# Performance work log

Measured on AMD Instinct MI355X. Metric: run time of the kernel, lower is better.

Reference implementation:

```python
import jax, jax.numpy as jnp
import numpy as np

N, H = 8192, 1024

def setup_inputs() -> dict:
    key = jax.random.key(0)
    ks = jax.random.split(key, 7)
    s = 1.0 / np.sqrt(H)
    return {
        "x": jax.random.normal(ks[0], (N, H), dtype=jnp.float32),
        "Wq": jax.random.uniform(ks[1], (H, H), dtype=jnp.float32, minval=-s, maxval=s),
        "bq": jax.random.uniform(ks[2], (H,), dtype=jnp.float32, minval=-s, maxval=s),
        "Wk": jax.random.uniform(ks[3], (H, H), dtype=jnp.float32, minval=-s, maxval=s),
        "bk": jax.random.uniform(ks[4], (H,), dtype=jnp.float32, minval=-s, maxval=s),
        "Wv": jax.random.uniform(ks[5], (H, H), dtype=jnp.float32, minval=-s, maxval=s),
        "bv": jax.random.uniform(ks[6], (H,), dtype=jnp.float32, minval=-s, maxval=s),
    }

def reference(x, Wq, bq, Wk, bk, Wv, bv):
    # q/k/v projections: [N, H]
    q = x @ Wq + bq
    k = x @ Wk + bk
    v = x @ Wv + bv
    # full scores [N, N]; NOTE: original has no 1/sqrt(d) scaling
    scores = q @ k.T
    alpha = jax.nn.softmax(scores, axis=1)
    return alpha @ v
```

## Files before the change

kernel.cpp:

```cpp
#include <hip/hip_runtime.h>
#include <hip/hip_bf16.h>
#include <hip/hip_fp16.h>


typedef _Float16 f16x8 __attribute__((ext_vector_type(8)));
typedef float floatx4 __attribute__((ext_vector_type(4)));
typedef float floatx2 __attribute__((ext_vector_type(2)));
typedef unsigned short ushortx8 __attribute__((ext_vector_type(8)));

__device__ __forceinline__ unsigned short f2h(float f) {
  __half h = __float2half(f);
  return __builtin_bit_cast(unsigned short, h);
}
__device__ __forceinline__ float h2f(unsigned short u) {
  return __half2float(__builtin_bit_cast(__half, u));
}

__device__ __forceinline__ void async16(const void* g, void* l) {
  __builtin_amdgcn_global_load_lds(
      (__attribute__((address_space(1))) unsigned int*)(g),
      (__attribute__((address_space(3))) unsigned int*)(l),
      16, 0, 0);
}


__global__ __launch_bounds__(256) void conv_f32_f16(const float* __restrict__ in,
                                                    unsigned short* __restrict__ out,
                                                    long n) {
  long i = ((long)blockIdx.x * 256 + threadIdx.x) * 4;
  if (i + 3 < n) {
    float4 f = *(const float4*)(in + i);
    ushort4 o;
    o.x = f2h(f.x); o.y = f2h(f.y); o.z = f2h(f.z); o.w = f2h(f.w);
    *(ushort4*)(out + i) = o;
  }
}

__global__ __launch_bounds__(256) void transpose_f32_f16_3(const float* __restrict__ in0,
                                                           const float* __restrict__ in1,
                                                           const float* __restrict__ in2,
                                                           unsigned short* __restrict__ out,
                                                           int rows, int cols) {
  const float* in = (blockIdx.z == 0) ? in0 : (blockIdx.z == 1) ? in1 : in2;
  unsigned short* o = out + (size_t)blockIdx.z * rows * cols;
  __shared__ float tile[32][33];
  int bx = blockIdx.x * 32;
  int by = blockIdx.y * 32;
  int tx = threadIdx.x & 31, ty = threadIdx.x >> 5;
  #pragma unroll
  for (int yy = ty; yy < 32; yy += 8)
    tile[yy][tx] = in[(size_t)(by + yy) * cols + bx + tx];
  __syncthreads();
  #pragma unroll
  for (int yy = ty; yy < 32; yy += 8)
    o[(size_t)(bx + yy) * rows + by + tx] = f2h(tile[tx][yy]);
}

__global__ __launch_bounds__(256, 4)
void gemm_bt(const unsigned short* __restrict__ A,
             const unsigned short* __restrict__ B,
             int M, int Nn, int K,
             const float* __restrict__ b0, const float* __restrict__ b1,
             const float* __restrict__ b2,
             unsigned short* __restrict__ out) {
  B   += (size_t)blockIdx.z * Nn * K;
  out += (size_t)blockIdx.z * M * Nn;
  const float* bias = (blockIdx.z == 0) ? b0 : (blockIdx.z == 1) ? b1 : b2;
  __shared__ unsigned short smem[128 * 136];
  unsigned short* As = smem;
  unsigned short* Bs = smem + 128 * 32;
  const int tid  = threadIdx.x;
  const int wave = tid >> 6;
  const int lane = tid & 63;
  const int wm = wave >> 1, wn = wave & 1;
  const int quad = lane >> 4, l16 = lane & 15;
  const long bm = (long)blockIdx.y * 128;
  const long bn = (long)blockIdx.x * 128;

  floatx4 acc[4][4] = {};

  const int srow = wave * 32 + (lane >> 2);
  const int scol = (lane & 3) * 8;
  const unsigned short* gA0 = A + (bm + srow) * (long)K + scol;
  const unsigned short* gA1 = gA0 + 16L * K;
  const unsigned short* gB0 = B + (bn + srow) * (long)K + scol;
  const unsigned short* gB1 = gB0 + 16L * K;
  unsigned short* lA0 = &As[(wave * 32) * 32];
  unsigned short* lA1 = &As[(wave * 32 + 16) * 32];
  unsigned short* lB0 = &Bs[(wave * 32) * 32];
  unsigned short* lB1 = &Bs[(wave * 32 + 16) * 32];

  for (int kk = 0; kk < K; kk += 32) {
    async16(gA0 + kk, lA0);
    async16(gA1 + kk, lA1);
    async16(gB0 + kk, lB0);
    async16(gB1 + kk, lB1);
    __syncthreads();
    f16x8 af[4], bfv[4];
    #pragma unroll
    for (int i = 0; i < 4; ++i) {
      af[i]  = *reinterpret_cast<const f16x8*>(&As[(wm * 64 + i * 16 + l16) * 32 + quad * 8]);
      bfv[i] = *reinterpret_cast<const f16x8*>(&Bs[(wn * 64 + i * 16 + l16) * 32 + quad * 8]);
    }
    #pragma unroll
    for (int i = 0; i < 4; ++i)
      #pragma unroll
      for (int j = 0; j < 4; ++j)
        acc[i][j] = __builtin_amdgcn_mfma_f32_16x16x32_f16(af[i], bfv[j], acc[i][j], 0, 0, 0);
    __syncthreads();
  }
  #pragma unroll
  for (int i = 0; i < 4; ++i) {
    const int row0 = wm * 64 + i * 16 + quad * 4;
    #pragma unroll
    for (int j = 0; j < 4; ++j) {
      const int col = wn * 64 + j * 16 + l16;
      const float cb = bias[bn + col];
      #pragma unroll
      for (int r = 0; r < 4; ++r)
        smem[(row0 + r) * 136 + col] = f2h(acc[i][j][r] + cb);
    }
  }
  __syncthreads();
  #pragma unroll
  for (int u = 0; u < 8; ++u) {
    const int chunk = u * 256 + tid;
    const int row = chunk >> 4;
    const int cc = chunk & 15;
    const ushortx8 val = *reinterpret_cast<const ushortx8*>(&smem[row * 136 + cc * 8]);
    *reinterpret_cast<ushortx8*>(&out[(bm + row) * (long)Nn + bn + cc * 8]) = val;
  }
}

__global__ __launch_bounds__(512, 2)
void gemm256(const unsigned short* __restrict__ A,
             const unsigned short* __restrict__ B,
             unsigned short* __restrict__ out) {
  constexpr int Nd = 8192;
  constexpr int K = 1024;
  __shared__ unsigned short smem[65536];
  const int tid  = threadIdx.x;
  const int lane = tid & 63;
  const int wave = tid >> 6;
  const int wm = wave >> 2, wn = wave & 3;
  const int quad = lane >> 4, l16 = lane & 15;

  const unsigned lin = blockIdx.y * gridDim.x + blockIdx.x;
  const unsigned nb  = gridDim.x * gridDim.y;
  const unsigned swz = (lin & 7u) * (nb >> 3) + (lin >> 3);
  const long bm = (long)(swz >> 5) * 256;
  const long bn = (long)(swz & 31u) * 256;

  floatx4 acc[8][4] = {};

  const int c0 = tid, c1 = tid + 512;
  const int r0 = c0 >> 2, r1 = c1 >> 2;
  const int sl0 = (c0 & 3) ^ ((r0 >> 1) & 3);
  const int sl1 = (c1 & 3) ^ ((r1 >> 1) & 3);
  const unsigned short* gA0 = A + (bm + r0) * (long)K + sl0 * 8;
  const unsigned short* gA1 = A + (bm + r1) * (long)K + sl1 * 8;
  const unsigned short* gB0 = B + (bn + r0) * (long)K + sl0 * 8;
  const unsigned short* gB1 = B + (bn + r1) * (long)K + sl1 * 8;
  const int ldsw0 = (c0 & ~63) * 8;
  const int ldsw1 = (c1 & ~63) * 8;

  auto STAGE = [&](int kt) {
    unsigned short* bufA = smem + (kt & 3) * 16384;
    unsigned short* bufB = bufA + 8192;
    const int ko = kt * 32;
    async16(gA0 + ko, bufA + ldsw0);
    async16(gA1 + ko, bufA + ldsw1);
    async16(gB0 + ko, bufB + ldsw0);
    async16(gB1 + ko, bufB + ldsw1);
  };

  STAGE(0); STAGE(1); STAGE(2);

  for (int kt = 0; kt < 32; ++kt) {
    const unsigned short* bufA = smem + (kt & 3) * 16384;
    const unsigned short* bufB = bufA + 8192;
    if (kt <= 29)      asm volatile("s_waitcnt vmcnt(8)" ::: "memory");
    else if (kt == 30) asm volatile("s_waitcnt vmcnt(4)" ::: "memory");
    else               asm volatile("s_waitcnt vmcnt(0)" ::: "memory");
    __builtin_amdgcn_s_barrier();
    __builtin_amdgcn_sched_barrier(0);
    if (kt + 3 < 32) STAGE(kt + 3);

    f16x8 bf[4];
    #pragma unroll
    for (int j = 0; j < 4; ++j) {
      const int R = wn * 64 + j * 16 + l16;
      bf[j] = *reinterpret_cast<const f16x8*>(
          bufB + R * 32 + ((quad ^ ((R >> 1) & 3)) * 8));
    }
    #pragma unroll
    for (int qd = 0; qd < 4; ++qd) {
      const int R0 = wm * 128 + (2 * qd) * 16 + l16;
      const int R1 = R0 + 16;
      const f16x8 a0 = *reinterpret_cast<const f16x8*>(
          bufA + R0 * 32 + ((quad ^ ((R0 >> 1) & 3)) * 8));
      const f16x8 a1 = *reinterpret_cast<const f16x8*>(
          bufA + R1 * 32 + ((quad ^ ((R1 >> 1) & 3)) * 8));
      __builtin_amdgcn_s_setprio(1);
      #pragma unroll
      for (int j = 0; j < 4; ++j) {
        acc[2 * qd][j] =
            __builtin_amdgcn_mfma_f32_16x16x32_f16(a0, bf[j], acc[2 * qd][j], 0, 0, 0);
        acc[2 * qd + 1][j] =
            __builtin_amdgcn_mfma_f32_16x16x32_f16(a1, bf[j], acc[2 * qd + 1][j], 0, 0, 0);
      }
      __builtin_amdgcn_s_setprio(0);
    }
  }

  __syncthreads();
  #pragma unroll
  for (int half = 0; half < 2; ++half) {
    if (wm == half) {
      #pragma unroll
      for (int i = 0; i < 8; ++i)
        #pragma unroll
        for (int j = 0; j < 4; ++j)
          #pragma unroll
          for (int r = 0; r < 4; ++r)
            smem[(i * 16 + quad * 4 + r) * 258 + wn * 64 + j * 16 + l16] =
                f2h(acc[i][j][r]);
    }
    __syncthreads();
    #pragma unroll
    for (int s = 0; s < 8; ++s) {
      const int chunk = s * 512 + tid;
      const int row = chunk >> 5, cc = chunk & 31;
      *reinterpret_cast<ushortx8*>(
          out + (bm + half * 128 + row) * (long)Nd + bn + cc * 8) =
          *reinterpret_cast<const ushortx8*>(smem + row * 258 + cc * 8);
    }
    __syncthreads();
  }
}

__global__ __launch_bounds__(256) void softmax_compact(unsigned short* __restrict__ S,
                                                       int* __restrict__ nnz, int n) {
  const int wid  = threadIdx.x >> 6;
  const int lane = threadIdx.x & 63;
  const int row  = blockIdx.x * 4 + wid;
  unsigned short* prow = S + ((size_t)row << 13);

  ushortx8 c[16];
  #pragma unroll
  for (int u = 0; u < 16; ++u)
    c[u] = *reinterpret_cast<const ushortx8*>(&prow[u * 512 + lane * 8]);

  float m0 = -1e30f, m1 = -1e30f, m2 = -1e30f, m3 = -1e30f;
  #pragma unroll
  for (int u = 0; u < 16; ++u) {
    m0 = fmaxf(m0, fmaxf(h2f(c[u][0]), h2f(c[u][4])));
    m1 = fmaxf(m1, fmaxf(h2f(c[u][1]), h2f(c[u][5])));
    m2 = fmaxf(m2, fmaxf(h2f(c[u][2]), h2f(c[u][6])));
    m3 = fmaxf(m3, fmaxf(h2f(c[u][3]), h2f(c[u][7])));
  }
  float m = fmaxf(fmaxf(m0, m1), fmaxf(m2, m3));
  #pragma unroll
  for (int off = 32; off > 0; off >>= 1)
    m = fmaxf(m, __shfl_xor(m, off, 64));

  float s0 = 0.f, s1 = 0.f, s2 = 0.f, s3 = 0.f;
  #pragma unroll
  for (int u = 0; u < 16; ++u) {
    s0 += __expf(h2f(c[u][0]) - m) + __expf(h2f(c[u][4]) - m);
    s1 += __expf(h2f(c[u][1]) - m) + __expf(h2f(c[u][5]) - m);
    s2 += __expf(h2f(c[u][2]) - m) + __expf(h2f(c[u][6]) - m);
    s3 += __expf(h2f(c[u][3]) - m) + __expf(h2f(c[u][7]) - m);
  }
  float s = (s0 + s1) + (s2 + s3);
  #pragma unroll
  for (int off = 32; off > 0; off >>= 1)
    s += __shfl_xor(s, off, 64);
  const float inv = 1.0f / s;

  unsigned int* pairs = (unsigned int*)prow;
  const int cap = 4096 - 8;
  int base = 0;
  #pragma unroll
  for (int u = 0; u < 16; ++u) {
    #pragma unroll
    for (int e = 0; e < 8; ++e) {
      const unsigned short hh = f2h(__expf(h2f(c[u][e]) - m) * inv);
      const unsigned long long mask = __ballot(hh != 0);
      if (hh) {
        const int pos = base + (int)__popcll(mask & ((1ull << lane) - 1ull));
        if (pos < cap)
          pairs[pos] = ((unsigned)(u * 512 + lane * 8 + e) << 16) | hh;
      }
      base += (int)__popcll(mask);
    }
  }
  const int c_cl = base < cap ? base : cap;
  const int padded = (c_cl + 7) & ~7;
  if (lane < padded - c_cl) pairs[c_cl + lane] = 0u;
  if (lane == 0) nnz[row] = padded;
}

__global__ __launch_bounds__(256) void pv_sliced(const unsigned short* __restrict__ S,
                                                 const int* __restrict__ nnz,
                                                 const unsigned short* __restrict__ v,
                                                 float* __restrict__ out,
                                                 int n) {
  const int wave = threadIdx.x >> 6;
  const int lane = threadIdx.x & 63;
  const int colbase = blockIdx.x * 128 + lane * 2;
  const unsigned colbyte = (unsigned)colbase * 2;
  const char* __restrict__ vb = (const char*)v;
  const char* __restrict__ sb = (const char*)S;

  #pragma unroll 1
  for (int r = 0; r < 4; ++r) {
    const int row = blockIdx.y + ((wave << 2) + r) * 512;
    int craw = nnz[row];
    craw = craw < 0 ? 0 : (craw > 4096 ? 4096 : craw);
    const int cnt = __builtin_amdgcn_readfirstlane(craw);
    const unsigned rowbase = (unsigned)row << 14;
    const unsigned pend = rowbase + 16384 - 32;
    unsigned poff = rowbase;
    uint4 q0 = *(const uint4*)(sb + poff);
    uint4 q1 = *(const uint4*)(sb + poff + 16);
    float a0 = 0.f, a1 = 0.f;
    for (int j = 0; j < cnt; j += 8) {
      const unsigned pn = (poff + 32 <= pend) ? poff + 32 : pend;
      const uint4 n0 = *(const uint4*)(sb + pn);
      const uint4 n1 = *(const uint4*)(sb + pn + 16);
      const unsigned p[8] = {q0.x, q0.y, q0.z, q0.w, q1.x, q1.y, q1.z, q1.w};
      #pragma unroll
      for (int u = 0; u < 8; ++u) {
        const ushort2 vv = *(const ushort2*)(vb + (((p[u] & 0xffff0000u) >> 5) + colbyte));
        const float w = h2f((unsigned short)(p[u] & 0xffffu));
        a0 += w * h2f(vv.x);
        a1 += w * h2f(vv.y);
      }
      q0 = n0; q1 = n1; poff = pn;
    }
    floatx2 o = {a0, a1};
    __builtin_nontemporal_store(o, (floatx2*)(out + ((size_t)row << 10) + colbase));
  }
}

extern "C" void kernel_launch(void* const* d_in, const int* in_sizes, int n_in,
                              void* d_out, int out_size, void* d_ws, size_t ws_size,
                              hipStream_t stream) {
  const int N = 8192, H = 1024;
  const float* x  = (const float*)d_in[0];
  const float* Wq = (const float*)d_in[1];
  const float* bq = (const float*)d_in[2];
  const float* Wk = (const float*)d_in[3];
  const float* bk = (const float*)d_in[4];
  const float* Wv = (const float*)d_in[5];
  const float* bv = (const float*)d_in[6];

  char* p = (char*)d_ws;
  unsigned short* xh  = (unsigned short*)p; p += (size_t)N * H * 2;
  unsigned short* WT  = (unsigned short*)p; p += (size_t)3 * H * H * 2;
  unsigned short* qkv = (unsigned short*)p; p += (size_t)3 * N * H * 2;
  unsigned short* S   = (unsigned short*)p; p += (size_t)N * N * 2;
  int*            nnz = (int*)p;            p += (size_t)N * 4;
  if ((size_t)(p - (char*)d_ws) > ws_size) return;
  unsigned short* qh = qkv;
  unsigned short* kh = qkv + (size_t)N * H;
  unsigned short* vh = qkv + (size_t)2 * N * H;

  conv_f32_f16<<<(N * H / 4 + 255) / 256, 256, 0, stream>>>(x, xh, (long)N * H);
  transpose_f32_f16_3<<<dim3(H / 32, H / 32, 3), 256, 0, stream>>>(Wq, Wk, Wv, WT, H, H);

  gemm_bt<<<dim3(H / 128, N / 128, 3), 256, 0, stream>>>(xh, WT, N, H, H,
                                                         bq, bk, bv, qkv);

  gemm256<<<dim3(N / 256, N / 256), 512, 0, stream>>>(qh, kh, S);

  softmax_compact<<<N / 4, 256, 0, stream>>>(S, nnz, N);
  pv_sliced<<<dim3(8, N / 16), 256, 0, stream>>>(S, nnz, vh, (float*)d_out, N);
}
```

Baseline: 552.6 us.

## Split GEMM k-step into two barrier-separated halves with staggered A/B prefetch

Splits each k-iteration's MFMA work into two halves of four M-fragments. The A and B async global-to-LDS loads are issued separately, one before each half, and the waits and barriers are moved to the end of the iteration. This aims to interleave LDS reads, global loads and MFMA bursts across waves, ping-pong style, to hide memory latency. It adds extra barriers per iteration and relies on the asm waitcnt accounting staying correct.

```diff
diff --git a/kernel.cpp b/kernel.cpp
--- a/kernel.cpp
+++ b/kernel.cpp
@@ -164,29 +164,31 @@
   const int ldsw0 = (c0 & ~63) * 8;
   const int ldsw1 = (c1 & ~63) * 8;
 
-  auto STAGE = [&](int kt) {
+  auto STAGE_A = [&](int kt) {
     unsigned short* bufA = smem + (kt & 3) * 16384;
-    unsigned short* bufB = bufA + 8192;
     const int ko = kt * 32;
     async16(gA0 + ko, bufA + ldsw0);
     async16(gA1 + ko, bufA + ldsw1);
+  };
+  auto STAGE_B = [&](int kt) {
+    unsigned short* bufB = smem + (kt & 3) * 16384 + 8192;
+    const int ko = kt * 32;
     async16(gB0 + ko, bufB + ldsw0);
     async16(gB1 + ko, bufB + ldsw1);
   };
 
-  STAGE(0); STAGE(1); STAGE(2);
+  STAGE_A(0); STAGE_B(0);
+  STAGE_A(1); STAGE_B(1);
+  STAGE_A(2); STAGE_B(2);
+  asm volatile("s_waitcnt vmcnt(8)" ::: "memory");
+  asm volatile("s_barrier" ::: "memory");
 
   for (int kt = 0; kt < 32; ++kt) {
     const unsigned short* bufA = smem + (kt & 3) * 16384;
     const unsigned short* bufB = bufA + 8192;
-    if (kt <= 29)      asm volatile("s_waitcnt vmcnt(8)" ::: "memory");
-    else if (kt == 30) asm volatile("s_waitcnt vmcnt(4)" ::: "memory");
-    else               asm volatile("s_waitcnt vmcnt(0)" ::: "memory");
-    __builtin_amdgcn_s_barrier();
-    __builtin_amdgcn_sched_barrier(0);
-    if (kt + 3 < 32) STAGE(kt + 3);
-
-    f16x8 bf[4];
+
+    if (kt + 3 < 32) STAGE_A(kt + 3);
+    f16x8 bf[4], af[4];
     #pragma unroll
     for (int j = 0; j < 4; ++j) {
       const int R = wn * 64 + j * 16 + l16;
@@ -194,23 +196,44 @@
           bufB + R * 32 + ((quad ^ ((R >> 1) & 3)) * 8));
     }
     #pragma unroll
-    for (int qd = 0; qd < 4; ++qd) {
-      const int R0 = wm * 128 + (2 * qd) * 16 + l16;
-      const int R1 = R0 + 16;
-      const f16x8 a0 = *reinterpret_cast<const f16x8*>(
-          bufA + R0 * 32 + ((quad ^ ((R0 >> 1) & 3)) * 8));
-      const f16x8 a1 = *reinterpret_cast<const f16x8*>(
-          bufA + R1 * 32 + ((quad ^ ((R1 >> 1) & 3)) * 8));
-      __builtin_amdgcn_s_setprio(1);
-      #pragma unroll
-      for (int j = 0; j < 4; ++j) {
-        acc[2 * qd][j] =
-            __builtin_amdgcn_mfma_f32_16x16x32_f16(a0, bf[j], acc[2 * qd][j], 0, 0, 0);
-        acc[2 * qd + 1][j] =
-            __builtin_amdgcn_mfma_f32_16x16x32_f16(a1, bf[j], acc[2 * qd + 1][j], 0, 0, 0);
-      }
-      __builtin_amdgcn_s_setprio(0);
-    }
+    for (int mf = 0; mf < 4; ++mf) {
+      const int R = wm * 128 + mf * 16 + l16;
+      af[mf] = *reinterpret_cast<const f16x8*>(
+          bufA + R * 32 + ((quad ^ ((R >> 1) & 3)) * 8));
+    }
+    asm volatile("s_barrier" ::: "memory");
+    __builtin_amdgcn_s_setprio(1);
+    #pragma unroll
+    for (int mf = 0; mf < 4; ++mf)
+      #pragma unroll
+      for (int j = 0; j < 4; ++j)
+        acc[mf][j] =
+            __builtin_amdgcn_mfma_f32_16x16x32_f16(af[mf], bf[j], acc[mf][j], 0, 0, 0);
+    __builtin_amdgcn_s_setprio(0);
+    asm volatile("s_barrier" ::: "memory");
+
+    if (kt + 3 < 32) STAGE_B(kt + 3);
+    f16x8 ag[4];
+    #pragma unroll
+    for (int mf = 0; mf < 4; ++mf) {
+      const int R = wm * 128 + (mf + 4) * 16 + l16;
+      ag[mf] = *reinterpret_cast<const f16x8*>(
+          bufA + R * 32 + ((quad ^ ((R >> 1) & 3)) * 8));
+    }
+    asm volatile("s_barrier" ::: "memory");
+    __builtin_amdgcn_s_setprio(1);
+    #pragma unroll
+    for (int mf = 0; mf < 4; ++mf)
+      #pragma unroll
+      for (int j = 0; j < 4; ++j)
+        acc[mf + 4][j] =
+            __builtin_amdgcn_mfma_f32_16x16x32_f16(ag[mf], bf[j], acc[mf + 4][j], 0, 0, 0);
+    __builtin_amdgcn_s_setprio(0);
+
+    if (kt <= 28)      asm volatile("s_waitcnt vmcnt(8)" ::: "memory");
+    else if (kt == 29) asm volatile("s_waitcnt vmcnt(4)" ::: "memory");
+    else if (kt == 30) asm volatile("s_waitcnt vmcnt(0)" ::: "memory");
+    asm volatile("s_barrier" ::: "memory");
   }
 
   __syncthreads();
```

After: 554.2 us. Within noise of the previous version (+0.3%).
